# Kernel tuning notes

Hardware: AMD Instinct MI355X
Metric: run time of the kernel (lower is better)

## Reference

```python
import jax, jax.numpy as jnp
import numpy as np

NEG_SLOPE = 0.2  # PyG GATConv default leaky_relu slope
EPS = 1e-16


def gat_conv(x, W, att_src, att_dst, bias, src, dst, num_nodes, heads, out_ch, concat):
    # x: [N, F_in]; W: [F_in, heads*out_ch]
    h = (x @ W).reshape(num_nodes, heads, out_ch)          # [N, H, C]
    a_src = jnp.sum(h * att_src, axis=-1)                  # [N, H]
    a_dst = jnp.sum(h * att_dst, axis=-1)                  # [N, H]
    alpha = jax.nn.leaky_relu(a_src[src] + a_dst[dst], NEG_SLOPE)  # [E, H]
    # segment softmax over incoming edges of each destination node
    amax = jax.ops.segment_max(alpha, dst, num_segments=num_nodes)  # [N, H]
    ex = jnp.exp(alpha - amax[dst])                        # [E, H]
    denom = jax.ops.segment_sum(ex, dst, num_segments=num_nodes)    # [N, H]
    attn = ex / (denom[dst] + EPS)                         # [E, H]
    msg = h[src] * attn[:, :, None]                        # [E, H, C]
    out = jax.ops.segment_sum(msg, dst, num_segments=num_nodes)     # [N, H, C]
    if concat:
        out = out.reshape(num_nodes, heads * out_ch)
    else:
        out = out.mean(axis=1)
    return out + bias


def setup_inputs() -> dict:
    key = jax.random.key(0)
    ks = jax.random.split(key, 10)
    N, E, F_in, H, C, OUT = 50000, 800000, 512, 4, 64, 40
    x = jax.random.normal(ks[0], (N, F_in), dtype=jnp.float32)
    edge_index = jax.random.randint(ks[1], (2, E), 0, N, dtype=jnp.int64)
    s1 = (2.0 / (F_in + H * C)) ** 0.5
    s2 = (2.0 / (H * C + OUT)) ** 0.5
    return {
        "x": x,
        "edge_index": edge_index,
        "W1": jax.random.normal(ks[2], (F_in, H * C), dtype=jnp.float32) * s1,
        "att_src1": jax.random.normal(ks[3], (H, C), dtype=jnp.float32) * 0.1,
        "att_dst1": jax.random.normal(ks[4], (H, C), dtype=jnp.float32) * 0.1,
        "b1": jnp.zeros((H * C,), dtype=jnp.float32),
        "W2": jax.random.normal(ks[5], (H * C, OUT), dtype=jnp.float32) * s2,
        "att_src2": jax.random.normal(ks[6], (1, OUT), dtype=jnp.float32) * 0.1,
        "att_dst2": jax.random.normal(ks[7], (1, OUT), dtype=jnp.float32) * 0.1,
        "b2": jnp.zeros((OUT,), dtype=jnp.float32),
    }


def reference(x, edge_index, W1, att_src1, att_dst1, b1, W2, att_src2, att_dst2, b2):
    N = x.shape[0]
    H, C = att_src1.shape
    OUT = att_src2.shape[1]
    # PyG GATConv default: add self-loops
    loops = jnp.arange(N, dtype=edge_index.dtype)
    src = jnp.concatenate([edge_index[0], loops])
    dst = jnp.concatenate([edge_index[1], loops])
    # dropout is identity in eval mode
    h = gat_conv(x, W1, att_src1, att_dst1, b1, src, dst, N, H, C, concat=True)
    h = jax.nn.elu(h)
    out = gat_conv(h, W2, att_src2, att_dst2, b2, src, dst, N, 1, OUT, concat=False)
    return jax.nn.log_softmax(out, axis=1)
```

## Files before the change

kernel.cpp:

```cpp
#include <hip/hip_runtime.h>
#include <math.h>

#define FIN   512
#define H1DIM 256
#define HEADS 4
#define CH    64
#define OUTC  40
#define NEG   0.2f
#define EPSV  1e-16f
#define BK    64

__device__ __forceinline__ float leaky(float a) { return a > 0.f ? a : NEG * a; }

__device__ __forceinline__ short f2bf(float f) {
    unsigned u = __builtin_bit_cast(unsigned, f);
    u += 0x7FFFu + ((u >> 16) & 1u);
    return (short)(u >> 16);
}
__device__ __forceinline__ float bf2f(short s) {
    return __builtin_bit_cast(float, ((unsigned)(unsigned short)s) << 16);
}

typedef __attribute__((ext_vector_type(8))) short short8;
typedef __attribute__((ext_vector_type(4))) short short4_t;
typedef __attribute__((ext_vector_type(4))) float float4_t;

typedef unsigned int u32;
typedef const __attribute__((address_space(1))) u32 gu32;
typedef __attribute__((address_space(3))) u32 lu32;

__device__ __forceinline__ void load_lds16(const void* g, void* l) {
    __builtin_amdgcn_global_load_lds((gu32*)g, (lu32*)l, 16, 0, 0);
}

__global__ void cvt_w1_kernel(const float* __restrict__ W1, short* __restrict__ w1t)
{
    int idx = blockIdx.x * 256 + threadIdx.x;
    if (idx >= FIN * H1DIM) return;
    int k = idx >> 8;
    int n = idx & 255;
    w1t[(size_t)n * FIN + k] = f2bf(W1[idx]);
}

__global__ __launch_bounds__(256) void gemm1_mfma_kernel(
    const float* __restrict__ x, const short* __restrict__ w1t,
    const float* __restrict__ attS, const float* __restrict__ attD,
    short* __restrict__ h1b, float* __restrict__ aS1, float* __restrict__ aD1, int N)
{
    __shared__ float Alf[64 * BK];
    __shared__ short Bls[256 * BK];

    const int tid  = threadIdx.x;
    const int lane = tid & 63;
    const int wid  = tid >> 6;
    const int row0 = blockIdx.x * 64;
    const int col0 = wid * 64;
    const int quad = lane >> 4;
    const int m16  = lane & 15;

    const int achunk = ((tid & 15) ^ (tid >> 4)) * 4;
    const float* asrcA[4];
#pragma unroll
    for (int p = 0; p < 4; ++p) {
        int r = row0 + p * 16 + (tid >> 4);
        if (r >= N) r = N - 1;
        asrcA[p] = x + (size_t)r * FIN + achunk;
    }

    const int trow = tid >> 3;
    const int bswz = ((tid & 7) ^ (trow & 7)) * 8;
    const short* bsrc[8];
#pragma unroll
    for (int p = 0; p < 8; ++p)
        bsrc[p] = w1t + (size_t)(p * 32 + trow) * FIN + bswz;

    float4_t acc[4][4];
#pragma unroll
    for (int i = 0; i < 4; ++i)
#pragma unroll
        for (int j = 0; j < 4; ++j) acc[i][j] = (float4_t){0.f, 0.f, 0.f, 0.f};

    const int swzB = (m16 & 7);

    for (int k0 = 0; k0 < FIN; k0 += BK) {
#pragma unroll
        for (int p = 0; p < 4; ++p)
            load_lds16(asrcA[p] + k0, Alf + p * 1024 + tid * 4);
#pragma unroll
        for (int p = 0; p < 8; ++p)
            load_lds16(bsrc[p] + k0, Bls + p * 2048 + tid * 8);
        __syncthreads();

#pragma unroll
        for (int half = 0; half < 2; ++half) {
            short8 a[4], b[4];
#pragma unroll
            for (int i = 0; i < 4; ++i) {
                int row = i * 16 + m16;
                int c0 = (quad + 4 * half) * 2;
                float4 f0 = *(const float4*)&Alf[row * BK + ((c0 ^ m16) * 4)];
                float4 f1 = *(const float4*)&Alf[row * BK + (((c0 + 1) ^ m16) * 4)];
                short8 t;
                t[0] = f2bf(f0.x); t[1] = f2bf(f0.y); t[2] = f2bf(f0.z); t[3] = f2bf(f0.w);
                t[4] = f2bf(f1.x); t[5] = f2bf(f1.y); t[6] = f2bf(f1.z); t[7] = f2bf(f1.w);
                a[i] = t;
            }
#pragma unroll
            for (int j = 0; j < 4; ++j) {
                int col = col0 + j * 16 + m16;
                int sub = (quad + 4 * half) ^ swzB;
                b[j] = *(const short8*)&Bls[col * BK + sub * 8];
            }
#pragma unroll
            for (int i = 0; i < 4; ++i)
#pragma unroll
                for (int j = 0; j < 4; ++j)
                    acc[i][j] = __builtin_amdgcn_mfma_f32_16x16x32_bf16(a[i], b[j], acc[i][j], 0, 0, 0);
        }
        __syncthreads();
    }

    float attSv[4], attDv[4];
#pragma unroll
    for (int j = 0; j < 4; ++j) {
        attSv[j] = attS[col0 + j * 16 + m16];
        attDv[j] = attD[col0 + j * 16 + m16];
    }

#pragma unroll
    for (int i = 0; i < 4; ++i) {
#pragma unroll
        for (int r = 0; r < 4; ++r) {
            int row = row0 + i * 16 + quad * 4 + r;
            if (row < N) {
#pragma unroll
                for (int j = 0; j < 4; ++j)
                    h1b[(size_t)row * H1DIM + col0 + j * 16 + m16] = f2bf(acc[i][j][r]);
            }
            float ps = acc[i][0][r] * attSv[0] + acc[i][1][r] * attSv[1]
                     + acc[i][2][r] * attSv[2] + acc[i][3][r] * attSv[3];
            float pd = acc[i][0][r] * attDv[0] + acc[i][1][r] * attDv[1]
                     + acc[i][2][r] * attDv[2] + acc[i][3][r] * attDv[3];
#pragma unroll
            for (int off = 1; off < 16; off <<= 1) {
                ps += __shfl_xor(ps, off);
                pd += __shfl_xor(pd, off);
            }
            if (m16 == 0 && row < N) {
                aS1[(size_t)row * 4 + wid] = ps;
                aD1[(size_t)row * 4 + wid] = pd;
            }
        }
    }
}

__global__ void degcount_kernel(const int* __restrict__ ei, int* __restrict__ deg,
                                int E, int Etot)
{
    int e = blockIdx.x * 256 + threadIdx.x;
    if (e >= Etot) return;
    int d = (e < E) ? ei[E + e] : (e - E);
    atomicAdd(&deg[d], 1);
}

__global__ __launch_bounds__(1024) void scan_partial_kernel(
    const int* __restrict__ deg, int* __restrict__ offsets,
    int* __restrict__ bsums, int N)
{
    __shared__ int wsums[16];
    __shared__ int excl[16];
    int tid = threadIdx.x, lane = tid & 63, wid = tid >> 6;
    int idx = blockIdx.x * 1024 + tid;
    int v = (idx < N) ? deg[idx] : 0;
    int sv = v;
#pragma unroll
    for (int off = 1; off < 64; off <<= 1) {
        int t = __shfl_up(sv, off, 64);
        if (lane >= off) sv += t;
    }
    if (lane == 63) wsums[wid] = sv;
    __syncthreads();
    if (wid == 0 && lane < 16) {
        int wv = wsums[lane];
        int sw = wv;
#pragma unroll
        for (int off = 1; off < 16; off <<= 1) {
            int t = __shfl_up(sw, off, 64);
            if (lane >= off) sw += t;
        }
        excl[lane] = sw - wv;
        if (lane == 15) bsums[blockIdx.x] = sw;
    }
    __syncthreads();
    if (idx < N) offsets[idx + 1] = sv + excl[wid];
}

__global__ __launch_bounds__(1024) void scan_tops_kernel(
    int* __restrict__ bsums, int* __restrict__ boffs, int nb)
{
    __shared__ int wsums[16];
    __shared__ int excl[16];
    int tid = threadIdx.x, lane = tid & 63, wid = tid >> 6;
    int v = (tid < nb) ? bsums[tid] : 0;
    int sv = v;
#pragma unroll
    for (int off = 1; off < 64; off <<= 1) {
        int t = __shfl_up(sv, off, 64);
        if (lane >= off) sv += t;
    }
    if (lane == 63) wsums[wid] = sv;
    __syncthreads();
    if (wid == 0 && lane < 16) {
        int wv = wsums[lane];
        int sw = wv;
#pragma unroll
        for (int off = 1; off < 16; off <<= 1) {
            int t = __shfl_up(sw, off, 64);
            if (lane >= off) sw += t;
        }
        excl[lane] = sw - wv;
    }
    __syncthreads();
    if (tid < nb) boffs[tid] = sv + excl[wid] - v;
}

__global__ __launch_bounds__(1024) void scan_add_kernel(
    int* __restrict__ offsets, const int* __restrict__ boffs, int N)
{
    int idx = blockIdx.x * 1024 + threadIdx.x;
    if (idx == 0) offsets[0] = 0;
    if (idx < N) offsets[idx + 1] += boffs[blockIdx.x];
}

__global__ void scatter_kernel(const int* __restrict__ ei, const int* __restrict__ offsets,
                               int* __restrict__ cursor, int* __restrict__ csr_src,
                               int E, int Etot)
{
    int e = blockIdx.x * 256 + threadIdx.x;
    if (e >= Etot) return;
    int s, d;
    if (e < E) { s = ei[e]; d = ei[E + e]; }
    else       { s = e - E; d = s; }
    int pos = offsets[d] + atomicAdd(&cursor[d], 1);
    csr_src[pos] = s;
}

__global__ __launch_bounds__(256) void agg1_kernel(
    const short* __restrict__ h1b, const float* __restrict__ aS,
    const float* __restrict__ aD, const int* __restrict__ offsets,
    const int* __restrict__ csr_src, const float* __restrict__ b1,
    short* __restrict__ g1b, int N)
{
    int lane = threadIdx.x & 63, wid = threadIdx.x >> 6;
    int n = blockIdx.x * 4 + wid;
    if (n >= N) return;
    int start = offsets[n], end = offsets[n + 1];
    int h = lane >> 4;
    int cbase = lane * 4;
    float adh = aD[(size_t)n * 4 + h];

    float ac0 = 0.f, ac1 = 0.f, ac2 = 0.f, ac3 = 0.f, denom = 0.f;
    int p = start;
    for (; p + 4 <= end; p += 4) {
        int s0 = csr_src[p], s1 = csr_src[p + 1], s2 = csr_src[p + 2], s3 = csr_src[p + 3];
        float w0 = __expf(leaky(aS[(size_t)s0 * 4 + h] + adh));
        float w1 = __expf(leaky(aS[(size_t)s1 * 4 + h] + adh));
        float w2 = __expf(leaky(aS[(size_t)s2 * 4 + h] + adh));
        float w3 = __expf(leaky(aS[(size_t)s3 * 4 + h] + adh));
        short4_t r0 = *(const short4_t*)&h1b[(size_t)s0 * H1DIM + cbase];
        short4_t r1 = *(const short4_t*)&h1b[(size_t)s1 * H1DIM + cbase];
        short4_t r2 = *(const short4_t*)&h1b[(size_t)s2 * H1DIM + cbase];
        short4_t r3 = *(const short4_t*)&h1b[(size_t)s3 * H1DIM + cbase];
        denom += w0 + w1 + w2 + w3;
        ac0 += w0 * bf2f(r0[0]) + w1 * bf2f(r1[0]) + w2 * bf2f(r2[0]) + w3 * bf2f(r3[0]);
        ac1 += w0 * bf2f(r0[1]) + w1 * bf2f(r1[1]) + w2 * bf2f(r2[1]) + w3 * bf2f(r3[1]);
        ac2 += w0 * bf2f(r0[2]) + w1 * bf2f(r1[2]) + w2 * bf2f(r2[2]) + w3 * bf2f(r3[2]);
        ac3 += w0 * bf2f(r0[3]) + w1 * bf2f(r1[3]) + w2 * bf2f(r2[3]) + w3 * bf2f(r3[3]);
    }
    for (; p < end; ++p) {
        int s = csr_src[p];
        float w = __expf(leaky(aS[(size_t)s * 4 + h] + adh));
        short4_t r = *(const short4_t*)&h1b[(size_t)s * H1DIM + cbase];
        denom += w;
        ac0 += w * bf2f(r[0]);
        ac1 += w * bf2f(r[1]);
        ac2 += w * bf2f(r[2]);
        ac3 += w * bf2f(r[3]);
    }

    float invh = 1.f / (denom + EPSV);
    float4 bb = *(const float4*)&b1[cbase];
    float v0 = ac0 * invh + bb.x;
    float v1 = ac1 * invh + bb.y;
    float v2 = ac2 * invh + bb.z;
    float v3 = ac3 * invh + bb.w;
    v0 = v0 > 0.f ? v0 : expm1f(v0);
    v1 = v1 > 0.f ? v1 : expm1f(v1);
    v2 = v2 > 0.f ? v2 : expm1f(v2);
    v3 = v3 > 0.f ? v3 : expm1f(v3);
    short4_t o;
    o[0] = f2bf(v0); o[1] = f2bf(v1); o[2] = f2bf(v2); o[3] = f2bf(v3);
    *(short4_t*)&g1b[(size_t)n * H1DIM + cbase] = o;
}

__global__ __launch_bounds__(256) void gemm2_kernel(
    const short* __restrict__ g1b, const float* __restrict__ W2,
    const float* __restrict__ attS2, const float* __restrict__ attD2,
    short* __restrict__ h2b, float* __restrict__ aS2, float* __restrict__ aD2, int N)
{
    __shared__ float rows[4][8][256];
    int lane = threadIdx.x & 63, wid = threadIdx.x >> 6;
    int nbase = blockIdx.x * 32 + wid * 8;
    bool act = lane < OUTC;
    int cc = act ? lane : 0;
    float attS = act ? attS2[lane] : 0.f;
    float attD = act ? attD2[lane] : 0.f;

#pragma unroll
    for (int i = 0; i < 8; ++i) {
        int n = nbase + i;
        float4 v = make_float4(0.f, 0.f, 0.f, 0.f);
        if (n < N) {
            short4_t hv = *(const short4_t*)&g1b[(size_t)n * H1DIM + lane * 4];
            v = make_float4(bf2f(hv[0]), bf2f(hv[1]), bf2f(hv[2]), bf2f(hv[3]));
        }
        *(float4*)&rows[wid][i][lane * 4] = v;
    }

    float acc[8];
#pragma unroll
    for (int i = 0; i < 8; ++i) acc[i] = 0.f;

    for (int k = 0; k < H1DIM; k += 4) {
        float w0 = W2[(size_t)(k + 0) * OUTC + cc];
        float w1 = W2[(size_t)(k + 1) * OUTC + cc];
        float w2 = W2[(size_t)(k + 2) * OUTC + cc];
        float w3 = W2[(size_t)(k + 3) * OUTC + cc];
#pragma unroll
        for (int i = 0; i < 8; ++i) {
            float4 g = *(const float4*)&rows[wid][i][k];
            acc[i] += g.x * w0 + g.y * w1 + g.z * w2 + g.w * w3;
        }
    }

#pragma unroll
    for (int i = 0; i < 8; ++i) {
        int n = nbase + i;
        if (n >= N) continue;
        if (act) h2b[(size_t)n * OUTC + lane] = f2bf(acc[i]);
        float ts = act ? acc[i] * attS : 0.f;
        float td = act ? acc[i] * attD : 0.f;
#pragma unroll
        for (int off = 32; off > 0; off >>= 1) {
            ts += __shfl_xor(ts, off);
            td += __shfl_xor(td, off);
        }
        if (lane == 0) { aS2[n] = ts; aD2[n] = td; }
    }
}

__global__ __launch_bounds__(256) void agg2_kernel(
    const short* __restrict__ h2b, const float* __restrict__ aS2,
    const float* __restrict__ aD2, const int* __restrict__ offsets,
    const int* __restrict__ csr_src, const float* __restrict__ b2,
    float* __restrict__ out, int N)
{
    int lane = threadIdx.x & 63, wid = threadIdx.x >> 6;
    int n = blockIdx.x * 4 + wid;
    if (n >= N) return;
    int start = offsets[n], end = offsets[n + 1];
    bool act = lane < OUTC;
    int cc = act ? lane : 0;
    float ad = aD2[n];

    float acc = 0.f, denom = 0.f;
    int p = start;
    for (; p + 4 <= end; p += 4) {
        int s0 = csr_src[p], s1 = csr_src[p + 1], s2 = csr_src[p + 2], s3 = csr_src[p + 3];
        float w0 = __expf(leaky(aS2[s0] + ad));
        float w1 = __expf(leaky(aS2[s1] + ad));
        float w2 = __expf(leaky(aS2[s2] + ad));
        float w3 = __expf(leaky(aS2[s3] + ad));
        short v0 = h2b[(size_t)s0 * OUTC + cc];
        short v1 = h2b[(size_t)s1 * OUTC + cc];
        short v2 = h2b[(size_t)s2 * OUTC + cc];
        short v3 = h2b[(size_t)s3 * OUTC + cc];
        denom += w0 + w1 + w2 + w3;
        acc += w0 * bf2f(v0) + w1 * bf2f(v1) + w2 * bf2f(v2) + w3 * bf2f(v3);
    }
    for (; p < end; ++p) {
        int s = csr_src[p];
        float w = __expf(leaky(aS2[s] + ad));
        denom += w;
        acc += w * bf2f(h2b[(size_t)s * OUTC + cc]);
    }

    float v = acc / (denom + EPSV) + (act ? b2[lane] : 0.f);

    float vm = act ? v : -INFINITY;
#pragma unroll
    for (int off = 32; off > 0; off >>= 1) vm = fmaxf(vm, __shfl_xor(vm, off));
    float ex2 = act ? __expf(v - vm) : 0.f;
    float tot = ex2;
#pragma unroll
    for (int off = 32; off > 0; off >>= 1) tot += __shfl_xor(tot, off);
    float res = v - vm - __logf(tot);
    if (act) out[(size_t)n * OUTC + lane] = res;
}

extern "C" void kernel_launch(void* const* d_in, const int* in_sizes, int n_in,
                              void* d_out, int out_size, void* d_ws, size_t ws_size,
                              hipStream_t stream)
{
    const float* x     = (const float*)d_in[0];
    const int*   ei    = (const int*)d_in[1];
    const float* W1    = (const float*)d_in[2];
    const float* attS1 = (const float*)d_in[3];
    const float* attD1 = (const float*)d_in[4];
    const float* b1    = (const float*)d_in[5];
    const float* W2    = (const float*)d_in[6];
    const float* attS2 = (const float*)d_in[7];
    const float* attD2 = (const float*)d_in[8];
    const float* b2    = (const float*)d_in[9];
    float* out = (float*)d_out;

    const int N    = in_sizes[0] / FIN;
    const int E    = in_sizes[1] / 2;
    const int Etot = E + N;
    const int nb   = (N + 1023) / 1024;

    char* ws = (char*)d_ws;
    size_t off = 0;
    auto take = [&](size_t bytes) -> char* {
        char* p = ws + off;
        off = (off + bytes + 255) & ~(size_t)255;
        return p;
    };
    short* h1b     = (short*)take((size_t)N * H1DIM * 2);
    short* g1b     = (short*)take((size_t)N * H1DIM * 2);
    short* w1t     = (short*)take((size_t)FIN * H1DIM * 2);
    float* aS1     = (float*)take((size_t)N * 4 * 4);
    float* aD1     = (float*)take((size_t)N * 4 * 4);
    short* h2b     = (short*)take((size_t)N * OUTC * 2);
    float* aS2v    = (float*)take((size_t)N * 4);
    float* aD2v    = (float*)take((size_t)N * 4);
    int*   degcur  = (int*)take((size_t)2 * N * 4);
    int*   deg     = degcur;
    int*   cursor  = degcur + N;
    int*   offsets = (int*)take((size_t)(N + 1) * 4);
    int*   bsums   = (int*)take((size_t)nb * 4);
    int*   boffs   = (int*)take((size_t)nb * 4);
    int*   csr_src = (int*)take((size_t)Etot * 4);

    hipMemsetAsync(degcur, 0, (size_t)2 * N * 4, stream);

    cvt_w1_kernel<<<(FIN * H1DIM + 255) / 256, 256, 0, stream>>>(W1, w1t);
    gemm1_mfma_kernel<<<(N + 63) / 64, 256, 0, stream>>>(x, w1t, attS1, attD1, h1b, aS1, aD1, N);
    degcount_kernel<<<(Etot + 255) / 256, 256, 0, stream>>>(ei, deg, E, Etot);
    scan_partial_kernel<<<nb, 1024, 0, stream>>>(deg, offsets, bsums, N);
    scan_tops_kernel<<<1, 1024, 0, stream>>>(bsums, boffs, nb);
    scan_add_kernel<<<nb, 1024, 0, stream>>>(offsets, boffs, N);
    scatter_kernel<<<(Etot + 255) / 256, 256, 0, stream>>>(ei, offsets, cursor, csr_src, E, Etot);
    agg1_kernel<<<(N + 3) / 4, 256, 0, stream>>>(h1b, aS1, aD1, offsets, csr_src, b1, g1b, N);
    gemm2_kernel<<<(N + 31) / 32, 256, 0, stream>>>(g1b, W2, attS2, attD2, h2b, aS2v, aD2v, N);
    agg2_kernel<<<(N + 3) / 4, 256, 0, stream>>>(h2b, aS2v, aD2v, offsets, csr_src, b2, out, N);
}
```

Measured before the change: 433.3 us.

## Split agg1 wave into two half-waves processing edges with 16-byte gathers

The layer-1 aggregation kernel now has each half of a wave handle alternate edges, with each lane loading 8 bf16 channels (16 bytes) instead of 4. The two halves' partial sums are combined with a cross-half shuffle before the epilogue. This widens each gather and gives more independent loads in flight per wave, at the cost of one extra shuffle reduction and idle lanes in the epilogue. Separately, the GEMM's fp32-to-bf16 conversion and the epilogue now use the hardware packed-convert instruction, and leaky_relu becomes a fmax.

```diff
diff --git a/kernel.cpp b/kernel.cpp
--- a/kernel.cpp
+++ b/kernel.cpp
@@ -10,7 +10,7 @@
 #define EPSV  1e-16f
 #define BK    64
 
-__device__ __forceinline__ float leaky(float a) { return a > 0.f ? a : NEG * a; }
+__device__ __forceinline__ float leaky(float a) { return fmaxf(a, NEG * a); }
 
 __device__ __forceinline__ short f2bf(float f) {
     unsigned u = __builtin_bit_cast(unsigned, f);
@@ -19,6 +19,17 @@
 }
 __device__ __forceinline__ float bf2f(short s) {
     return __builtin_bit_cast(float, ((unsigned)(unsigned short)s) << 16);
+}
+__device__ __forceinline__ unsigned cvtpk(float lo, float hi) {
+    unsigned r;
+    asm("v_cvt_pk_bf16_f32 %0, %1, %2" : "=v"(r) : "v"(lo), "v"(hi));
+    return r;
+}
+__device__ __forceinline__ float lo16(unsigned u) {
+    return __builtin_bit_cast(float, u << 16);
+}
+__device__ __forceinline__ float hi16(unsigned u) {
+    return __builtin_bit_cast(float, u & 0xffff0000u);
 }
 
 typedef __attribute__((ext_vector_type(8))) short short8;
@@ -100,10 +111,11 @@
                 int c0 = (quad + 4 * half) * 2;
                 float4 f0 = *(const float4*)&Alf[row * BK + ((c0 ^ m16) * 4)];
                 float4 f1 = *(const float4*)&Alf[row * BK + (((c0 + 1) ^ m16) * 4)];
-                short8 t;
-                t[0] = f2bf(f0.x); t[1] = f2bf(f0.y); t[2] = f2bf(f0.z); t[3] = f2bf(f0.w);
-                t[4] = f2bf(f1.x); t[5] = f2bf(f1.y); t[6] = f2bf(f1.z); t[7] = f2bf(f1.w);
-                a[i] = t;
+                unsigned* tp = (unsigned*)&a[i];
+                tp[0] = cvtpk(f0.x, f0.y);
+                tp[1] = cvtpk(f0.z, f0.w);
+                tp[2] = cvtpk(f1.x, f1.y);
+                tp[3] = cvtpk(f1.z, f1.w);
             }
 #pragma unroll
             for (int j = 0; j < 4; ++j) {
@@ -252,55 +264,96 @@
     short* __restrict__ g1b, int N)
 {
     int lane = threadIdx.x & 63, wid = threadIdx.x >> 6;
+    int half = lane >> 5;
+    int l32  = lane & 31;
     int n = blockIdx.x * 4 + wid;
     if (n >= N) return;
     int start = offsets[n], end = offsets[n + 1];
-    int h = lane >> 4;
-    int cbase = lane * 4;
+    int h = l32 >> 3;
+    int cbase = l32 * 8;
     float adh = aD[(size_t)n * 4 + h];
 
-    float ac0 = 0.f, ac1 = 0.f, ac2 = 0.f, ac3 = 0.f, denom = 0.f;
+    float ac[8];
+#pragma unroll
+    for (int c = 0; c < 8; ++c) ac[c] = 0.f;
+    float denom = 0.f;
+
     int p = start;
     for (; p + 4 <= end; p += 4) {
-        int s0 = csr_src[p], s1 = csr_src[p + 1], s2 = csr_src[p + 2], s3 = csr_src[p + 3];
-        float w0 = __expf(leaky(aS[(size_t)s0 * 4 + h] + adh));
-        float w1 = __expf(leaky(aS[(size_t)s1 * 4 + h] + adh));
-        float w2 = __expf(leaky(aS[(size_t)s2 * 4 + h] + adh));
-        float w3 = __expf(leaky(aS[(size_t)s3 * 4 + h] + adh));
-        short4_t r0 = *(const short4_t*)&h1b[(size_t)s0 * H1DIM + cbase];
-        short4_t r1 = *(const short4_t*)&h1b[(size_t)s1 * H1DIM + cbase];
-        short4_t r2 = *(const short4_t*)&h1b[(size_t)s2 * H1DIM + cbase];
-        short4_t r3 = *(const short4_t*)&h1b[(size_t)s3 * H1DIM + cbase];
-        denom += w0 + w1 + w2 + w3;
-        ac0 += w0 * bf2f(r0[0]) + w1 * bf2f(r1[0]) + w2 * bf2f(r2[0]) + w3 * bf2f(r3[0]);
-        ac1 += w0 * bf2f(r0[1]) + w1 * bf2f(r1[1]) + w2 * bf2f(r2[1]) + w3 * bf2f(r3[1]);
-        ac2 += w0 * bf2f(r0[2]) + w1 * bf2f(r1[2]) + w2 * bf2f(r2[2]) + w3 * bf2f(r3[2]);
-        ac3 += w0 * bf2f(r0[3]) + w1 * bf2f(r1[3]) + w2 * bf2f(r2[3]) + w3 * bf2f(r3[3]);
-    }
-    for (; p < end; ++p) {
+        int sA0 = csr_src[p],     sB0 = csr_src[p + 1];
+        int sA1 = csr_src[p + 2], sB1 = csr_src[p + 3];
+        int s0 = half ? sB0 : sA0;
+        int s1 = half ? sB1 : sA1;
+        float t0 = aS[(size_t)s0 * 4 + h] + adh;
+        float t1 = aS[(size_t)s1 * 4 + h] + adh;
+        short8 r0 = *(const short8*)&h1b[(size_t)s0 * H1DIM + cbase];
+        short8 r1 = *(const short8*)&h1b[(size_t)s1 * H1DIM + cbase];
+        float w0 = __expf(leaky(t0));
+        float w1 = __expf(leaky(t1));
+        denom += w0 + w1;
+        const unsigned* u0 = (const unsigned*)&r0;
+        const unsigned* u1 = (const unsigned*)&r1;
+#pragma unroll
+        for (int k = 0; k < 4; ++k) {
+            ac[2 * k]     += w0 * lo16(u0[k]) + w1 * lo16(u1[k]);
+            ac[2 * k + 1] += w0 * hi16(u0[k]) + w1 * hi16(u1[k]);
+        }
+    }
+    for (; p + 2 <= end; p += 2) {
+        int sA = csr_src[p], sB = csr_src[p + 1];
+        int s = half ? sB : sA;
+        float t = aS[(size_t)s * 4 + h] + adh;
+        short8 r = *(const short8*)&h1b[(size_t)s * H1DIM + cbase];
+        float w = __expf(leaky(t));
+        denom += w;
+        const unsigned* u = (const unsigned*)&r;
+#pragma unroll
+        for (int k = 0; k < 4; ++k) {
+            ac[2 * k]     += w * lo16(u[k]);
+            ac[2 * k + 1] += w * hi16(u[k]);
+        }
+    }
+    if (p < end) {
         int s = csr_src[p];
-        float w = __expf(leaky(aS[(size_t)s * 4 + h] + adh));
-        short4_t r = *(const short4_t*)&h1b[(size_t)s * H1DIM + cbase];
+        float t = aS[(size_t)s * 4 + h] + adh;
+        short8 r = *(const short8*)&h1b[(size_t)s * H1DIM + cbase];
+        float w = half ? 0.f : __expf(leaky(t));
         denom += w;
-        ac0 += w * bf2f(r[0]);
-        ac1 += w * bf2f(r[1]);
-        ac2 += w * bf2f(r[2]);
-        ac3 += w * bf2f(r[3]);
-    }
-
-    float invh = 1.f / (denom + EPSV);
-    float4 bb = *(const float4*)&b1[cbase];
-    float v0 = ac0 * invh + bb.x;
-    float v1 = ac1 * invh + bb.y;
-    float v2 = ac2 * invh + bb.z;
-    float v3 = ac3 * invh + bb.w;
-    v0 = v0 > 0.f ? v0 : expm1f(v0);
-    v1 = v1 > 0.f ? v1 : expm1f(v1);
-    v2 = v2 > 0.f ? v2 : expm1f(v2);
-    v3 = v3 > 0.f ? v3 : expm1f(v3);
-    short4_t o;
-    o[0] = f2bf(v0); o[1] = f2bf(v1); o[2] = f2bf(v2); o[3] = f2bf(v3);
-    *(short4_t*)&g1b[(size_t)n * H1DIM + cbase] = o;
+        const unsigned* u = (const unsigned*)&r;
+#pragma unroll
+        for (int k = 0; k < 4; ++k) {
+            ac[2 * k]     += w * lo16(u[k]);
+            ac[2 * k + 1] += w * hi16(u[k]);
+        }
+    }
+
+    denom += __shfl_xor(denom, 32);
+#pragma unroll
+    for (int c = 0; c < 8; ++c) ac[c] += __shfl_xor(ac[c], 32);
+
+    if (half == 0) {
+        float inv = 1.f / (denom + EPSV);
+        float4 b0 = *(const float4*)&b1[cbase];
+        float4 b4 = *(const float4*)&b1[cbase + 4];
+        float v[8];
+        v[0] = ac[0] * inv + b0.x;
+        v[1] = ac[1] * inv + b0.y;
+        v[2] = ac[2] * inv + b0.z;
+        v[3] = ac[3] * inv + b0.w;
+        v[4] = ac[4] * inv + b4.x;
+        v[5] = ac[5] * inv + b4.y;
+        v[6] = ac[6] * inv + b4.z;
+        v[7] = ac[7] * inv + b4.w;
+#pragma unroll
+        for (int c = 0; c < 8; ++c) v[c] = v[c] > 0.f ? v[c] : expm1f(v[c]);
+        short8 o;
+        unsigned* op = (unsigned*)&o;
+        op[0] = cvtpk(v[0], v[1]);
+        op[1] = cvtpk(v[2], v[3]);
+        op[2] = cvtpk(v[4], v[5]);
+        op[3] = cvtpk(v[6], v[7]);
+        *(short8*)&g1b[(size_t)n * H1DIM + cbase] = o;
+    }
 }
 
 __global__ __launch_bounds__(256) void gemm2_kernel(
```

Result: no change. 433.2 us (-0.0%).
